# Kernel optimization log

Measured on AMD Instinct MI355X. Metric: run time of the kernel, lower is better.

## Reference

```python
import jax, jax.numpy as jnp
import numpy as np

B, S, H, I, E, TOP_K = 2, 1024, 1024, 2048, 8, 2


def setup_inputs() -> dict:
    key = jax.random.key(0)
    k1, k2, k3, k4 = jax.random.split(key, 4)
    return {
        "hidden_states": jax.random.normal(k1, (B, S, H), dtype=jnp.float32),
        "gate_weight": jax.random.normal(k2, (E, H), dtype=jnp.float32) * 0.02,
        "gate_up_proj": jax.random.normal(k3, (E, 2 * I, H), dtype=jnp.float32) * 0.02,
        "down_proj": jax.random.normal(k4, (E, H, I), dtype=jnp.float32) * 0.02,
    }


def reference(hidden_states, gate_weight, gate_up_proj, down_proj):
    b, s, h = hidden_states.shape
    T = b * s
    x = hidden_states.reshape(T, h)

    # --- router ---
    router_logits = x @ gate_weight.T                          # [T, E]
    router_probs = jax.nn.softmax(router_logits.astype(jnp.float32), axis=-1)
    router_probs = router_probs.astype(router_logits.dtype)
    top_vals, top_idx = jax.lax.top_k(router_probs, TOP_K)     # [T, K]
    # norm_topk_prob = True
    routing_weights = top_vals / jnp.maximum(top_vals.sum(-1, keepdims=True), 1e-12)

    # --- dense all-expert FFN ---
    gu = jnp.einsum('th,eoh->eto', x, gate_up_proj)            # [E, T, 2I]
    gate_h, up_h = jnp.split(gu, 2, axis=-1)
    inter = jax.nn.silu(gate_h) * up_h                          # [E, T, I]
    expert_out = jnp.einsum('eti,ehi->eth', inter, down_proj).astype(jnp.float32)  # [E, T, H]

    # --- pairwise Frobenius similarity (sim = 1 - dist/max_dist, diag=1) ---
    flat = expert_out.reshape(E, -1)
    gram = flat @ flat.T                                        # [E, E]
    sq = jnp.diagonal(gram)
    dist = jnp.sqrt(jnp.clip(sq[:, None] + sq[None, :] - 2.0 * gram, 0.0))
    dist = dist.at[jnp.arange(E), jnp.arange(E)].set(0.0)
    sim = 1.0 - dist / jnp.maximum(dist.max(), 1e-12)
    sim = sim.at[jnp.arange(E), jnp.arange(E)].set(1.0)

    # --- top-k weighted combine (gather along expert axis) ---
    gathered = expert_out[top_idx, jnp.arange(T)[:, None]]      # [T, K, H]
    final = (gathered * routing_weights[..., None].astype(jnp.float32)).sum(axis=1)
    final = final.astype(hidden_states.dtype).reshape(b, s, h)
    return final, sim
```

## Files before the change

kernel.cpp:

```cpp
#include <hip/hip_runtime.h>
#include <math.h>

#define T_TOK 2048
#define H_DIM 1024
#define I_DIM 2048
#define NEXP  8

typedef _Float16 f16x8 __attribute__((ext_vector_type(8)));
typedef _Float16 f16x4 __attribute__((ext_vector_type(4)));
typedef float    f32x4 __attribute__((ext_vector_type(4)));

__device__ __forceinline__ void cp16(const void* g, void* l) {
  __builtin_amdgcn_global_load_lds(
      (const __attribute__((address_space(1))) void*)g,
      (__attribute__((address_space(3))) void*)l, 16, 0, 0);
}

__global__ __launch_bounds__(256) void cvt_f16_kernel(
    const float* __restrict__ in, _Float16* __restrict__ hi, int n) {
  int i = (blockIdx.x * 256 + threadIdx.x) * 4;
  if (i >= n) return;
  float4 v = *(const float4*)(in + i);
  f16x4 hv = {(_Float16)v.x, (_Float16)v.y, (_Float16)v.z, (_Float16)v.w};
  *(f16x4*)(hi + i) = hv;
}

__global__ __launch_bounds__(64) void router_kernel(
    const float* __restrict__ x, const float* __restrict__ gw,
    int* __restrict__ topIdx, float* __restrict__ topW) {
  int t = blockIdx.x;
  int lane = threadIdx.x;
  float p[NEXP];
#pragma unroll
  for (int e = 0; e < NEXP; ++e) p[e] = 0.f;
  const float* xr = x + (size_t)t * H_DIM;
  for (int h = lane; h < H_DIM; h += 64) {
    float xv = xr[h];
#pragma unroll
    for (int e = 0; e < NEXP; ++e) p[e] += xv * gw[e * H_DIM + h];
  }
#pragma unroll
  for (int e = 0; e < NEXP; ++e) {
    float v = p[e];
    for (int off = 32; off > 0; off >>= 1) v += __shfl_down(v, off);
    p[e] = v;
  }
  if (lane == 0) {
    float mx = p[0];
#pragma unroll
    for (int e = 1; e < NEXP; ++e) mx = fmaxf(mx, p[e]);
    float ex[NEXP], s = 0.f;
#pragma unroll
    for (int e = 0; e < NEXP; ++e) { ex[e] = expf(p[e] - mx); s += ex[e]; }
#pragma unroll
    for (int e = 0; e < NEXP; ++e) ex[e] /= s;
    int i0 = 0; float v0 = ex[0];
#pragma unroll
    for (int e = 1; e < NEXP; ++e) if (ex[e] > v0) { v0 = ex[e]; i0 = e; }
    int i1 = -1; float v1 = -1.f;
#pragma unroll
    for (int e = 0; e < NEXP; ++e) if (e != i0 && ex[e] > v1) { v1 = ex[e]; i1 = e; }
    float sum = fmaxf(v0 + v1, 1e-12f);
    topIdx[2 * t] = i0;  topIdx[2 * t + 1] = i1;
    topW[2 * t] = v0 / sum;  topW[2 * t + 1] = v1 / sum;
  }
}

__global__ __launch_bounds__(256, 2) void gemm_gateup(
    const _Float16* __restrict__ xHi, const _Float16* __restrict__ gup16,
    _Float16* __restrict__ intHi) {
  __shared__ _Float16 lds[24576];

  const int tid = threadIdx.x;
  const int wave = tid >> 6, lane = tid & 63;
  const int rowA0 = blockIdx.y * 128;
  const int colB0 = blockIdx.x * 128;
  const int e = blockIdx.z;

  const int sr = lane >> 3;
  const int sc = lane & 7;
  const int gcol = (sc ^ sr) * 8;
  const int rbase = wave * 8 + sr;

  const int wm = wave >> 1, wn = wave & 1;
  const int fr = lane & 15;
  const int quad = lane >> 4;

  f32x4 accG[4][4], accU[4][4];
#pragma unroll
  for (int i = 0; i < 4; ++i)
#pragma unroll
    for (int j = 0; j < 4; ++j) {
      accG[i][j] = (f32x4){0.f, 0.f, 0.f, 0.f};
      accU[i][j] = (f32x4){0.f, 0.f, 0.f, 0.f};
    }

  const _Float16* gupG = gup16 + ((size_t)e * 2 * I_DIM + colB0) * H_DIM;
  const _Float16* gupU = gupG + (size_t)I_DIM * H_DIM;
  char* ldsB = (char*)lds;

  for (int k0 = 0; k0 < H_DIM; k0 += 64) {
    const int kcol = k0 + gcol;
#pragma unroll
    for (int i = 0; i < 4; ++i) {
      const int row = i * 32 + rbase;
      const unsigned dst = (unsigned)(i * 4096 + wave * 1024);
      cp16(xHi  + (size_t)(rowA0 + row) * H_DIM + kcol, ldsB + dst);
      cp16(gupG + (size_t)row * H_DIM + kcol, ldsB + 16384u + dst);
      cp16(gupU + (size_t)row * H_DIM + kcol, ldsB + 32768u + dst);
    }
    __syncthreads();

#pragma unroll
    for (int kk = 0; kk < 2; ++kk) {
      f16x8 ah[4];
#pragma unroll
      for (int i = 0; i < 4; ++i) {
        const int row = wm * 64 + i * 16 + fr;
        ah[i] = *(const f16x8*)&lds[row * 64 + (((kk * 4 + quad) ^ (fr & 7)) * 8)];
      }
#pragma unroll
      for (int j = 0; j < 4; ++j) {
        const int row = wn * 64 + j * 16 + fr;
        const int boff = row * 64 + (((kk * 4 + quad) ^ (fr & 7)) * 8);
        f16x8 bg = *(const f16x8*)&lds[8192 + boff];
        f16x8 bu = *(const f16x8*)&lds[16384 + boff];
#pragma unroll
        for (int i = 0; i < 4; ++i) {
          accG[i][j] = __builtin_amdgcn_mfma_f32_16x16x32_f16(ah[i], bg, accG[i][j], 0, 0, 0);
          accU[i][j] = __builtin_amdgcn_mfma_f32_16x16x32_f16(ah[i], bu, accU[i][j], 0, 0, 0);
        }
      }
    }
    __syncthreads();
  }

  const int er = quad * 4;
  const int ec = lane & 15;
#pragma unroll
  for (int i = 0; i < 4; ++i)
#pragma unroll
    for (int j = 0; j < 4; ++j) {
      const int row = rowA0 + wm * 64 + i * 16 + er;
      const int col = colB0 + wn * 64 + j * 16 + ec;
#pragma unroll
      for (int r = 0; r < 4; ++r) {
        float g = accG[i][j][r], u = accU[i][j][r];
        float val = g / (1.f + __expf(-g)) * u;
        intHi[((size_t)e * T_TOK + row + r) * I_DIM + col] = (_Float16)val;
      }
    }
}

__global__ __launch_bounds__(256, 4) void gemm_down(
    const _Float16* __restrict__ intHi, const _Float16* __restrict__ wd16,
    _Float16* __restrict__ eo) {
  __shared__ _Float16 lds[16384];

  const int tid = threadIdx.x;
  const int wave = tid >> 6, lane = tid & 63;
  const int rowA0 = blockIdx.x * 128;
  const int colB0 = blockIdx.y * 128;
  const int e = blockIdx.z;

  const int sr = lane >> 3;
  const int sc = lane & 7;
  const int gcol = (sc ^ sr) * 8;
  const int rbase = wave * 8 + sr;

  const int wm = wave >> 1, wn = wave & 1;
  const int fr = lane & 15;
  const int quad = lane >> 4;

  f32x4 acc[4][4];
#pragma unroll
  for (int i = 0; i < 4; ++i)
#pragma unroll
    for (int j = 0; j < 4; ++j) acc[i][j] = (f32x4){0.f, 0.f, 0.f, 0.f};

  const _Float16* aBase = intHi + (size_t)e * T_TOK * I_DIM;
  const _Float16* bBase = wd16 + ((size_t)e * H_DIM + colB0) * I_DIM;
  char* ldsB = (char*)lds;

  for (int k0 = 0; k0 < I_DIM; k0 += 64) {
    const int kcol = k0 + gcol;
#pragma unroll
    for (int i = 0; i < 4; ++i) {
      const int row = i * 32 + rbase;
      const unsigned dst = (unsigned)(i * 4096 + wave * 1024);
      cp16(aBase + (size_t)(rowA0 + row) * I_DIM + kcol, ldsB + dst);
      cp16(bBase + (size_t)row * I_DIM + kcol, ldsB + 16384u + dst);
    }
    __syncthreads();

#pragma unroll
    for (int kk = 0; kk < 2; ++kk) {
      f16x8 ah[4];
#pragma unroll
      for (int i = 0; i < 4; ++i) {
        const int row = wm * 64 + i * 16 + fr;
        ah[i] = *(const f16x8*)&lds[row * 64 + (((kk * 4 + quad) ^ (fr & 7)) * 8)];
      }
#pragma unroll
      for (int j = 0; j < 4; ++j) {
        const int row = wn * 64 + j * 16 + fr;
        const int boff = row * 64 + (((kk * 4 + quad) ^ (fr & 7)) * 8);
        f16x8 bh = *(const f16x8*)&lds[8192 + boff];
#pragma unroll
        for (int i = 0; i < 4; ++i)
          acc[i][j] = __builtin_amdgcn_mfma_f32_16x16x32_f16(ah[i], bh, acc[i][j], 0, 0, 0);
      }
    }
    __syncthreads();
  }

  const int er = quad * 4;
  const int ec = lane & 15;
#pragma unroll
  for (int i = 0; i < 4; ++i)
#pragma unroll
    for (int j = 0; j < 4; ++j) {
      const int row = rowA0 + wm * 64 + i * 16 + er;
      const int col = colB0 + wn * 64 + j * 16 + ec;
#pragma unroll
      for (int r = 0; r < 4; ++r)
        eo[((size_t)e * T_TOK + row + r) * H_DIM + col] = (_Float16)acc[i][j][r];
    }
}

__global__ __launch_bounds__(256) void gram_kernel(
    const _Float16* __restrict__ eo, float* __restrict__ gram) {
  float s[36];
#pragma unroll
  for (int p = 0; p < 36; ++p) s[p] = 0.f;
  const size_t total = (size_t)T_TOK * H_DIM;
  const size_t stride = (size_t)gridDim.x * 256;
  for (size_t j = (size_t)blockIdx.x * 256 + threadIdx.x; j < total; j += stride) {
    float v[NEXP];
#pragma unroll
    for (int e = 0; e < NEXP; ++e) v[e] = (float)eo[(size_t)e * total + j];
    int p = 0;
#pragma unroll
    for (int a = 0; a < NEXP; ++a)
#pragma unroll
      for (int b = a; b < NEXP; ++b) { s[p] += v[a] * v[b]; ++p; }
  }
#pragma unroll
  for (int p = 0; p < 36; ++p) {
    float v = s[p];
    for (int off = 32; off > 0; off >>= 1) v += __shfl_down(v, off);
    s[p] = v;
  }
  __shared__ float red[4][36];
  const int wave = threadIdx.x >> 6, lane = threadIdx.x & 63;
  if (lane == 0)
#pragma unroll
    for (int p = 0; p < 36; ++p) red[wave][p] = s[p];
  __syncthreads();
  if (threadIdx.x < 36) {
    float v = red[0][threadIdx.x] + red[1][threadIdx.x] + red[2][threadIdx.x] + red[3][threadIdx.x];
    atomicAdd(&gram[threadIdx.x], v);
  }
}

__global__ __launch_bounds__(64) void sim_kernel(
    const float* __restrict__ gram, float* __restrict__ simOut) {
  const int t = threadIdx.x;
  const int e1 = t >> 3, e2 = t & 7;
  int a = e1 < e2 ? e1 : e2;
  int b = e1 < e2 ? e2 : e1;
  const float g = gram[a * 8 - a * (a - 1) / 2 + (b - a)];
  const float sq1 = gram[e1 * 8 - e1 * (e1 - 1) / 2];
  const float sq2 = gram[e2 * 8 - e2 * (e2 - 1) / 2];
  float d2 = fmaxf(sq1 + sq2 - 2.f * g, 0.f);
  float dist = (e1 == e2) ? 0.f : sqrtf(d2);
  float dmax = dist;
  for (int off = 32; off > 0; off >>= 1) dmax = fmaxf(dmax, __shfl_xor(dmax, off));
  float sim = 1.f - dist / fmaxf(dmax, 1e-12f);
  if (e1 == e2) sim = 1.f;
  simOut[t] = sim;
}

__global__ __launch_bounds__(256) void final_kernel(
    const _Float16* __restrict__ eo, const int* __restrict__ topIdx,
    const float* __restrict__ topW, float* __restrict__ out) {
  const int t = blockIdx.x;
  const int c = threadIdx.x * 4;
  const int i0 = topIdx[2 * t], i1 = topIdx[2 * t + 1];
  const float w0 = topW[2 * t], w1 = topW[2 * t + 1];
  const size_t per = (size_t)T_TOK * H_DIM;
  f16x4 a = *(const f16x4*)&eo[(size_t)i0 * per + (size_t)t * H_DIM + c];
  f16x4 b = *(const f16x4*)&eo[(size_t)i1 * per + (size_t)t * H_DIM + c];
  float4 r;
  r.x = w0 * (float)a[0] + w1 * (float)b[0];
  r.y = w0 * (float)a[1] + w1 * (float)b[1];
  r.z = w0 * (float)a[2] + w1 * (float)b[2];
  r.w = w0 * (float)a[3] + w1 * (float)b[3];
  *(float4*)&out[(size_t)t * H_DIM + c] = r;
}

extern "C" void kernel_launch(void* const* d_in, const int* in_sizes, int n_in,
                              void* d_out, int out_size, void* d_ws, size_t ws_size,
                              hipStream_t stream) {
  (void)in_sizes; (void)n_in; (void)out_size; (void)ws_size;
  const float* x   = (const float*)d_in[0];
  const float* gw  = (const float*)d_in[1];
  const float* gup = (const float*)d_in[2];
  const float* dwn = (const float*)d_in[3];
  float* out = (float*)d_out;

  char* ws = (char*)d_ws;
  const size_t MB = 1u << 20;
  _Float16* xHi    = (_Float16*)(ws + 0 * MB);
  _Float16* intHi  = (_Float16*)(ws + 4 * MB);
  _Float16* gup16  = (_Float16*)(ws + 68 * MB);
  _Float16* wd16   = (_Float16*)(ws + 68 * MB);
  _Float16* eo     = (_Float16*)(ws + 100 * MB);
  int*      topIdx = (int*)(ws + 132 * MB);
  float*    topW   = (float*)(ws + 132 * MB + 16384);
  float*    gram   = (float*)(ws + 132 * MB + 32768);

  cvt_f16_kernel<<<2048, 256, 0, stream>>>(x, xHi, T_TOK * H_DIM);
  cvt_f16_kernel<<<32768, 256, 0, stream>>>(gup, gup16, NEXP * 2 * I_DIM * H_DIM);
  router_kernel<<<T_TOK, 64, 0, stream>>>(x, gw, topIdx, topW);
  hipMemsetAsync(gram, 0, 36 * sizeof(float), stream);

  gemm_gateup<<<dim3(I_DIM / 128, T_TOK / 128, NEXP), 256, 0, stream>>>(
      xHi, gup16, intHi);

  cvt_f16_kernel<<<16384, 256, 0, stream>>>(dwn, wd16, NEXP * H_DIM * I_DIM);

  gemm_down<<<dim3(T_TOK / 128, H_DIM / 128, NEXP), 256, 0, stream>>>(
      intHi, wd16, eo);

  gram_kernel<<<2048, 256, 0, stream>>>(eo, gram);
  sim_kernel<<<1, 64, 0, stream>>>(gram, out + (size_t)T_TOK * H_DIM);
  final_kernel<<<T_TOK, 256, 0, stream>>>(eo, topIdx, topW, out);
}
```

Measured before the change: 506.9 us.

## Enlarge down-proj GEMM tile to 256x256 with double-buffered LDS prefetch

The down-projection GEMM moves from 128x128 tiles with 4 waves to 256x256 tiles with 8 waves. It double-buffers the LDS loads so the next K-slice's global-to-LDS copies overlap the current slice's MFMAs, and it raises wave priority around the MFMA burst. This aims to increase data reuse per LDS byte and hide load latency. In exchange it uses 128 KB of LDS and more registers, so only one block fits per CU and occupancy is lower.

```diff
diff --git a/kernel.cpp b/kernel.cpp
--- a/kernel.cpp
+++ b/kernel.cpp
@@ -152,64 +152,83 @@
     }
 }
 
-__global__ __launch_bounds__(256, 4) void gemm_down(
+__global__ __launch_bounds__(512, 2) void gemm_down(
     const _Float16* __restrict__ intHi, const _Float16* __restrict__ wd16,
     _Float16* __restrict__ eo) {
-  __shared__ _Float16 lds[16384];
+  __shared__ _Float16 lds[65536];
 
   const int tid = threadIdx.x;
   const int wave = tid >> 6, lane = tid & 63;
-  const int rowA0 = blockIdx.x * 128;
-  const int colB0 = blockIdx.y * 128;
+  const int rowA0 = blockIdx.x * 256;
+  const int colB0 = blockIdx.y * 256;
   const int e = blockIdx.z;
 
   const int sr = lane >> 3;
   const int sc = lane & 7;
   const int gcol = (sc ^ sr) * 8;
-  const int rbase = wave * 8 + sr;
-
-  const int wm = wave >> 1, wn = wave & 1;
+
+  const int wm = wave >> 2;
+  const int wn = wave & 3;
   const int fr = lane & 15;
   const int quad = lane >> 4;
 
-  f32x4 acc[4][4];
-#pragma unroll
-  for (int i = 0; i < 4; ++i)
+  f32x4 acc[8][4];
+#pragma unroll
+  for (int i = 0; i < 8; ++i)
 #pragma unroll
     for (int j = 0; j < 4; ++j) acc[i][j] = (f32x4){0.f, 0.f, 0.f, 0.f};
 
-  const _Float16* aBase = intHi + (size_t)e * T_TOK * I_DIM;
-  const _Float16* bBase = wd16 + ((size_t)e * H_DIM + colB0) * I_DIM;
+  const _Float16* aSrc = intHi + (size_t)e * T_TOK * I_DIM +
+                         (size_t)(rowA0 + wave * 8 + sr) * I_DIM + gcol;
+  const _Float16* bSrc = wd16 + ((size_t)e * H_DIM + colB0 + wave * 8 + sr) * I_DIM + gcol;
   char* ldsB = (char*)lds;
-
-  for (int k0 = 0; k0 < I_DIM; k0 += 64) {
-    const int kcol = k0 + gcol;
-#pragma unroll
-    for (int i = 0; i < 4; ++i) {
-      const int row = i * 32 + rbase;
-      const unsigned dst = (unsigned)(i * 4096 + wave * 1024);
-      cp16(aBase + (size_t)(rowA0 + row) * I_DIM + kcol, ldsB + dst);
-      cp16(bBase + (size_t)row * I_DIM + kcol, ldsB + 16384u + dst);
-    }
-    __syncthreads();
-
-#pragma unroll
-    for (int kk = 0; kk < 2; ++kk) {
-      f16x8 ah[4];
-#pragma unroll
-      for (int i = 0; i < 4; ++i) {
-        const int row = wm * 64 + i * 16 + fr;
-        ah[i] = *(const f16x8*)&lds[row * 64 + (((kk * 4 + quad) ^ (fr & 7)) * 8)];
-      }
+  char* ldsAw = ldsB + wave * 1024u;
+  char* ldsBw = ldsAw + 32768u;
+
+  const int NT = I_DIM / 64;
+
+#pragma unroll
+  for (int s = 0; s < 4; ++s) {
+    cp16(aSrc + (size_t)s * 64 * I_DIM, ldsAw + s * 8192u);
+    cp16(bSrc + (size_t)s * 64 * I_DIM, ldsBw + s * 8192u);
+  }
+  __syncthreads();
+
+  for (int t = 0; t < NT; ++t) {
+    const int cur = t & 1;
+    if (t < NT - 1) {
+      const unsigned nb = (unsigned)((cur ^ 1) * 65536u);
+      const _Float16* aS = aSrc + (size_t)(t + 1) * 64;
+      const _Float16* bS = bSrc + (size_t)(t + 1) * 64;
+#pragma unroll
+      for (int s = 0; s < 4; ++s) {
+        cp16(aS + (size_t)s * 64 * I_DIM, ldsAw + nb + s * 8192u);
+        cp16(bS + (size_t)s * 64 * I_DIM, ldsBw + nb + s * 8192u);
+      }
+    }
+    const int cb = cur * 32768;
+#pragma unroll
+    for (int ks = 0; ks < 2; ++ks) {
+      const int ksl = (ks * 4 + quad);
+      f16x8 bh[4];
 #pragma unroll
       for (int j = 0; j < 4; ++j) {
         const int row = wn * 64 + j * 16 + fr;
-        const int boff = row * 64 + (((kk * 4 + quad) ^ (fr & 7)) * 8);
-        f16x8 bh = *(const f16x8*)&lds[8192 + boff];
-#pragma unroll
-        for (int i = 0; i < 4; ++i)
-          acc[i][j] = __builtin_amdgcn_mfma_f32_16x16x32_f16(ah[i], bh, acc[i][j], 0, 0, 0);
-      }
+        bh[j] = *(const f16x8*)&lds[cb + 16384 + row * 64 + ((ksl ^ (fr & 7)) * 8)];
+      }
+      f16x8 ah[8];
+#pragma unroll
+      for (int i = 0; i < 8; ++i) {
+        const int row = wm * 128 + i * 16 + fr;
+        ah[i] = *(const f16x8*)&lds[cb + row * 64 + ((ksl ^ (fr & 7)) * 8)];
+      }
+      __builtin_amdgcn_s_setprio(1);
+#pragma unroll
+      for (int j = 0; j < 4; ++j)
+#pragma unroll
+        for (int i = 0; i < 8; ++i)
+          acc[i][j] = __builtin_amdgcn_mfma_f32_16x16x32_f16(ah[i], bh[j], acc[i][j], 0, 0, 0);
+      __builtin_amdgcn_s_setprio(0);
     }
     __syncthreads();
   }
@@ -217,10 +236,10 @@
   const int er = quad * 4;
   const int ec = lane & 15;
 #pragma unroll
-  for (int i = 0; i < 4; ++i)
+  for (int i = 0; i < 8; ++i)
 #pragma unroll
     for (int j = 0; j < 4; ++j) {
-      const int row = rowA0 + wm * 64 + i * 16 + er;
+      const int row = rowA0 + wm * 128 + i * 16 + er;
       const int col = colB0 + wn * 64 + j * 16 + ec;
 #pragma unroll
       for (int r = 0; r < 4; ++r)
@@ -330,7 +349,7 @@
 
   cvt_f16_kernel<<<16384, 256, 0, stream>>>(dwn, wd16, NEXP * H_DIM * I_DIM);
 
-  gemm_down<<<dim3(T_TOK / 128, H_DIM / 128, NEXP), 256, 0, stream>>>(
+  gemm_down<<<dim3(T_TOK / 256, H_DIM / 256, NEXP), 512, 0, stream>>>(
       intHi, wd16, eo);
 
   gram_kernel<<<2048, 256, 0, stream>>>(eo, gram);
```

Result: no change. 513.6 us (+1.3%).
